# Kernel tuning notes

Measured on AMD Instinct MI355X. Metric: run time of the kernel, lower is better.

## Reference

```python
import jax, jax.numpy as jnp
import numpy as np

B, P, N, C, H, E, HORIZON = 4, 8, 10000, 64, 256, 160000, 4


def setup_inputs() -> dict:
    key = jax.random.key(0)
    ks = jax.random.split(key, 32)
    rn = lambda k, shape, s=0.05: jax.random.normal(k, shape, jnp.float32) * s
    inp = {
        "x_seq": rn(ks[0], (B, P, N, C), 1.0),
        "ei0": jax.random.randint(ks[1], (2, E), 0, N, dtype=jnp.int32),
        "ei1": jax.random.randint(ks[2], (2, E), 0, N, dtype=jnp.int32),
        "Wl0": rn(ks[3], (C, H)), "bl0": jnp.zeros((H,), jnp.float32), "Wr0": rn(ks[4], (C, H)),
        "Wl1": rn(ks[5], (C, H)), "bl1": jnp.zeros((H,), jnp.float32), "Wr1": rn(ks[6], (C, H)),
        "Wp": rn(ks[7], (C, H)), "bp": jnp.zeros((C,), jnp.float32),
    }
    i = 8
    for g in ("g1", "g2", "g3"):
        inp[g + "_Wih"] = rn(ks[i], (3 * H, H)); i += 1
        inp[g + "_Whh"] = rn(ks[i], (3 * H, H)); i += 1
        inp[g + "_bih"] = jnp.zeros((3 * H,), jnp.float32)
        inp[g + "_bhh"] = jnp.zeros((3 * H,), jnp.float32)
    return inp


def _sage(x, src, dst, Wl, bl, Wr, n_nodes):
    # PyG SAGEConv (mean aggr): lin_l(mean_j x_j) + lin_r(x_i); lin_r has no bias.
    agg = jax.ops.segment_sum(x[src], dst, num_segments=n_nodes)  # [n, C]
    cnt = jax.ops.segment_sum(jnp.ones((src.shape[0],), x.dtype), dst, num_segments=n_nodes)
    agg = agg / jnp.maximum(cnt, 1.0)[:, None]
    return agg @ Wl + bl + x @ Wr


def _gru(x, h, Wih, Whh, bih, bhh):
    gi = x @ Wih.T + bih
    gh = h @ Whh.T + bhh
    ir, iz, inn = jnp.split(gi, 3, axis=1)
    hr, hz, hn = jnp.split(gh, 3, axis=1)
    r = jax.nn.sigmoid(ir + hr)
    z = jax.nn.sigmoid(iz + hz)
    n = jnp.tanh(inn + r * hn)
    return (1.0 - z) * n + z * h


def reference(x_seq, ei0, ei1,
              Wl0, bl0, Wr0, Wl1, bl1, Wr1,
              g1_Wih, g1_Whh, g1_bih, g1_bhh,
              g2_Wih, g2_Whh, g2_bih, g2_bhh,
              g3_Wih, g3_Whh, g3_bih, g3_bhh,
              Wp, bp):
    Bn = B * N
    off = (jnp.arange(B) * N).astype(ei0.dtype)
    batch = lambda ei: (ei[:, None, :] + off[None, :, None]).reshape(2, -1)
    b0, b1 = batch(ei0), batch(ei1)

    def step(xt, h1, h2, h3):
        c = (_sage(xt, b0[0], b0[1], Wl0, bl0, Wr0, Bn)
             + _sage(xt, b1[0], b1[1], Wl1, bl1, Wr1, Bn))  # HeteroConv aggr='sum'
        c = jax.nn.relu(c)  # dropout is identity in eval
        h1 = _gru(c, h1, g1_Wih, g1_Whh, g1_bih, g1_bhh)
        h2 = _gru(h1, h2, g2_Wih, g2_Whh, g2_bih, g2_bhh)
        h3 = _gru(h2, h3, g3_Wih, g3_Whh, g3_bih, g3_bhh)
        return h1, h2, h3

    h0 = jnp.zeros((Bn, H), x_seq.dtype)
    xs = jnp.transpose(x_seq, (1, 0, 2, 3)).reshape(P, Bn, C)

    def enc_body(carry, xt):
        return step(xt, *carry), None

    (h1, h2, h3), _ = jax.lax.scan(enc_body, (h0, h0, h0), xs)

    def dec_body(carry, _):
        h1, h2, h3, xd = carry
        h1, h2, h3 = step(xd, h1, h2, h3)
        y = h3 @ Wp.T + bp  # [Bn, C]
        return (h1, h2, h3, y), y

    x_dec = x_seq[:, -1].reshape(Bn, C)
    _, ys = jax.lax.scan(dec_body, (h1, h2, h3, x_dec), None, length=HORIZON)
    # ys: [HORIZON, Bn, C] -> [B, HORIZON, N, C]
    return jnp.transpose(ys.reshape(HORIZON, B, N, C), (1, 0, 2, 3))
```

## Files before the change

kernel.cpp:

```cpp
#include <hip/hip_runtime.h>
#include <hip/hip_bf16.h>
#include <cstdint>

#define B_   4
#define P_   8
#define N_   10000
#define C_   64
#define H_   256
#define E_   160000
#define HOR_ 4
#define BN_  (B_ * N_)
#define MPAD 40064

typedef __bf16 bf16;
typedef __attribute__((ext_vector_type(8))) __bf16 bf16x8;
typedef __attribute__((ext_vector_type(4))) float f32x4;

__device__ __forceinline__ void gl2lds16(const bf16* g, bf16* l) {
    __builtin_amdgcn_global_load_lds(
        (const __attribute__((address_space(1))) void*)g,
        (__attribute__((address_space(3))) void*)l, 16, 0, 0);
}

template <int BIAS, int RELU, int OUTBF, int PROJ>
__global__ __launch_bounds__(256) void gemm_k(
    const bf16* __restrict__ A, const bf16* __restrict__ Bt,
    void* __restrict__ Cp, const float* __restrict__ bias,
    int K, int Nn, int tstep)
{
    __shared__ __align__(16) bf16 As[128 * 32];
    __shared__ __align__(16) bf16 Bs[128 * 32];

    const int tid  = threadIdx.x;
    const int m0   = blockIdx.y * 128;
    const int n0   = blockIdx.x * 128;
    const int wave = tid >> 6;
    const int lane = tid & 63;
    const int wm   = (wave >> 1) << 6;
    const int wn   = (wave & 1) << 6;
    const int lr   = lane & 15;
    const int kg   = lane >> 4;

    f32x4 acc[4][4] = {};

    const int r0 = tid >> 2;
    const int k0 = (tid & 3) << 3;

    for (int kk = 0; kk < K; kk += 32) {
        const bf16* ga = A  + (size_t)(m0 + r0) * K + kk + k0;
        const bf16* gb = Bt + (size_t)(n0 + r0) * K + kk + k0;
        gl2lds16(ga,                  As + tid * 8);
        gl2lds16(ga + 64 * (size_t)K, As + 2048 + tid * 8);
        gl2lds16(gb,                  Bs + tid * 8);
        gl2lds16(gb + 64 * (size_t)K, Bs + 2048 + tid * 8);
        __syncthreads();

        bf16x8 af[4], bfv[4];
#pragma unroll
        for (int i = 0; i < 4; ++i)
            af[i] = *reinterpret_cast<const bf16x8*>(&As[(wm + i * 16 + lr) * 32 + kg * 8]);
#pragma unroll
        for (int j = 0; j < 4; ++j)
            bfv[j] = *reinterpret_cast<const bf16x8*>(&Bs[(wn + j * 16 + lr) * 32 + kg * 8]);
#pragma unroll
        for (int i = 0; i < 4; ++i)
#pragma unroll
            for (int j = 0; j < 4; ++j)
                acc[i][j] = __builtin_amdgcn_mfma_f32_16x16x32_bf16(af[i], bfv[j], acc[i][j], 0, 0, 0);
        __syncthreads();
    }

#pragma unroll
    for (int i = 0; i < 4; ++i) {
#pragma unroll
        for (int j = 0; j < 4; ++j) {
#pragma unroll
            for (int v = 0; v < 4; ++v) {
                int row = m0 + wm + i * 16 + kg * 4 + v;
                int col = n0 + wn + j * 16 + lr;
                float val = acc[i][j][v];
                if (BIAS) val += bias[col];
                if (RELU) val = fmaxf(val, 0.f);
                if (PROJ) {
                    if (col < C_ && row < BN_) {
                        int b = row / N_, n = row - b * N_;
                        reinterpret_cast<float*>(Cp)[(((size_t)b * HOR_ + tstep) * N_ + n) * C_ + col] = val;
                    }
                } else if (OUTBF) {
                    reinterpret_cast<bf16*>(Cp)[(size_t)row * Nn + col] = (bf16)val;
                } else {
                    reinterpret_cast<float*>(Cp)[(size_t)row * Nn + col] = val;
                }
            }
        }
    }
}

__global__ __launch_bounds__(256, 2) void gru_fused_k(
    const bf16* __restrict__ X, const bf16* __restrict__ Hc,
    bf16* __restrict__ Hn,
    const bf16* __restrict__ Wih, const bf16* __restrict__ Whh,
    const float* __restrict__ bih, const float* __restrict__ bhh)
{
    const int id    = blockIdx.x;
    const int sblk  = id >> 6;
    const int jblk  = (id >> 3) & 7;
    const int slow  = id & 7;
    const int strip = (sblk << 3) | slow;
    if (strip >= 313) return;

    __shared__ __align__(16) bf16 Xs[128 * 32];
    __shared__ __align__(16) bf16 Hs[128 * 32];
    __shared__ __align__(16) bf16 Ws[6 * 32 * 32];

    const int tid  = threadIdx.x;
    const int m0   = strip * 128;
    const int j0   = jblk * 32;
    const int wave = tid >> 6;
    const int lane = tid & 63;
    const int wm   = (wave >> 1) << 6;
    const int wn   = (wave & 1) << 4;
    const int lr   = lane & 15;
    const int kg   = lane >> 4;

    f32x4 acc[4][4] = {};

    const int r0 = tid >> 2;
    const int k0 = (tid & 3) << 3;

    int wgate[3], wrow[3], wk[3];
#pragma unroll
    for (int c = 0; c < 3; ++c) {
        int f = c * 2048 + tid * 8;
        wgate[c] = f >> 10;
        wrow[c]  = (f >> 5) & 31;
        wk[c]    = f & 31;
    }

    for (int kk = 0; kk < 256; kk += 32) {
        gl2lds16(X  + (size_t)(m0 + r0) * 256 + kk + k0,      Xs + tid * 8);
        gl2lds16(X  + (size_t)(m0 + r0 + 64) * 256 + kk + k0, Xs + 2048 + tid * 8);
        gl2lds16(Hc + (size_t)(m0 + r0) * 256 + kk + k0,      Hs + tid * 8);
        gl2lds16(Hc + (size_t)(m0 + r0 + 64) * 256 + kk + k0, Hs + 2048 + tid * 8);
#pragma unroll
        for (int c = 0; c < 3; ++c) {
            int g = wgate[c];
            const bf16* src = (g < 3)
                ? Wih + (size_t)(g * 256 + j0 + wrow[c]) * 256 + kk + wk[c]
                : Whh + (size_t)((g - 3) * 256 + j0 + wrow[c]) * 256 + kk + wk[c];
            gl2lds16(src, Ws + c * 2048 + tid * 8);
        }
        __syncthreads();

        bf16x8 af[4], ah[4], bw[6];
#pragma unroll
        for (int i = 0; i < 4; ++i) {
            af[i] = *reinterpret_cast<const bf16x8*>(&Xs[(wm + i * 16 + lr) * 32 + kg * 8]);
            ah[i] = *reinterpret_cast<const bf16x8*>(&Hs[(wm + i * 16 + lr) * 32 + kg * 8]);
        }
#pragma unroll
        for (int g = 0; g < 6; ++g)
            bw[g] = *reinterpret_cast<const bf16x8*>(&Ws[g * 1024 + (wn + lr) * 32 + kg * 8]);
#pragma unroll
        for (int g = 0; g < 3; ++g)
#pragma unroll
            for (int i = 0; i < 4; ++i)
                acc[g][i] = __builtin_amdgcn_mfma_f32_16x16x32_bf16(af[i], bw[g], acc[g][i], 0, 0, 0);
#pragma unroll
        for (int i = 0; i < 4; ++i)
            acc[0][i] = __builtin_amdgcn_mfma_f32_16x16x32_bf16(ah[i], bw[3], acc[0][i], 0, 0, 0);
#pragma unroll
        for (int i = 0; i < 4; ++i)
            acc[1][i] = __builtin_amdgcn_mfma_f32_16x16x32_bf16(ah[i], bw[4], acc[1][i], 0, 0, 0);
#pragma unroll
        for (int i = 0; i < 4; ++i)
            acc[3][i] = __builtin_amdgcn_mfma_f32_16x16x32_bf16(ah[i], bw[5], acc[3][i], 0, 0, 0);
        __syncthreads();
    }

    const int col = j0 + wn + lr;
    const float b_r  = bih[col]       + bhh[col];
    const float b_z  = bih[256 + col] + bhh[256 + col];
    const float bi_n = bih[512 + col];
    const float bh_n = bhh[512 + col];
#pragma unroll
    for (int i = 0; i < 4; ++i) {
#pragma unroll
        for (int v = 0; v < 4; ++v) {
            int row = m0 + wm + i * 16 + kg * 4 + v;
            float r = __fdividef(1.f, 1.f + __expf(-(acc[0][i][v] + b_r)));
            float z = __fdividef(1.f, 1.f + __expf(-(acc[1][i][v] + b_z)));
            float a = (acc[2][i][v] + bi_n) + r * (acc[3][i][v] + bh_n);
            a = fminf(fmaxf(a, -15.f), 15.f);
            float t2 = __expf(2.f * a);
            float nn = __fdividef(t2 - 1.f, t2 + 1.f);
            float hold = (float)Hc[(size_t)row * 256 + col];
            Hn[(size_t)row * 256 + col] = (bf16)((1.f - z) * nn + z * hold);
        }
    }
}

struct __attribute__((aligned(8))) bf4 { bf16 b[4]; };

__global__ __launch_bounds__(256) void gather_conv_k(
    const float* __restrict__ xbase, long long sB, long long sN,
    const int* __restrict__ rp0, const int* __restrict__ col0,
    const int* __restrict__ rp1, const int* __restrict__ col1,
    bf16* __restrict__ Aconv)
{
    int wid  = (blockIdx.x * 256 + threadIdx.x) >> 6;
    int lane = threadIdx.x & 63;
    if (wid >= BN_) return;
    int b = wid / N_;
    int n = wid - b * N_;
    int eg = lane >> 4;
    int cl = lane & 15;
    const float* xb = xbase + (size_t)b * sB;

    float4 xv = *reinterpret_cast<const float4*>(&xb[(size_t)n * sN + cl * 4]);

    float4 s0 = {0.f, 0.f, 0.f, 0.f};
    int st = rp0[n], en = rp0[n + 1];
    float d0 = fmaxf((float)(en - st), 1.f);
    for (int e = st + eg; e < en; e += 4) {
        const float4 v = *reinterpret_cast<const float4*>(&xb[(size_t)col0[e] * sN + cl * 4]);
        s0.x += v.x; s0.y += v.y; s0.z += v.z; s0.w += v.w;
    }

    float4 s1 = {0.f, 0.f, 0.f, 0.f};
    st = rp1[n]; en = rp1[n + 1];
    float d1 = fmaxf((float)(en - st), 1.f);
    for (int e = st + eg; e < en; e += 4) {
        const float4 v = *reinterpret_cast<const float4*>(&xb[(size_t)col1[e] * sN + cl * 4]);
        s1.x += v.x; s1.y += v.y; s1.z += v.z; s1.w += v.w;
    }

#pragma unroll
    for (int m = 16; m <= 32; m <<= 1) {
        s0.x += __shfl_xor(s0.x, m, 64); s0.y += __shfl_xor(s0.y, m, 64);
        s0.z += __shfl_xor(s0.z, m, 64); s0.w += __shfl_xor(s0.w, m, 64);
        s1.x += __shfl_xor(s1.x, m, 64); s1.y += __shfl_xor(s1.y, m, 64);
        s1.z += __shfl_xor(s1.z, m, 64); s1.w += __shfl_xor(s1.w, m, 64);
    }

    if (eg == 0) {
        float r0 = 1.f / d0, r1 = 1.f / d1;
        bf16* row = Aconv + (size_t)wid * 192;
        bf4 o;
        o.b[0] = (bf16)(s0.x * r0); o.b[1] = (bf16)(s0.y * r0);
        o.b[2] = (bf16)(s0.z * r0); o.b[3] = (bf16)(s0.w * r0);
        *reinterpret_cast<bf4*>(&row[cl * 4]) = o;
        o.b[0] = (bf16)xv.x; o.b[1] = (bf16)xv.y; o.b[2] = (bf16)xv.z; o.b[3] = (bf16)xv.w;
        *reinterpret_cast<bf4*>(&row[64 + cl * 4]) = o;
        o.b[0] = (bf16)(s1.x * r1); o.b[1] = (bf16)(s1.y * r1);
        o.b[2] = (bf16)(s1.z * r1); o.b[3] = (bf16)(s1.w * r1);
        *reinterpret_cast<bf4*>(&row[128 + cl * 4]) = o;
    }
}

__global__ void count_k(const int* __restrict__ ei, int* __restrict__ cnt) {
    int e = blockIdx.x * 256 + threadIdx.x;
    if (e < E_) atomicAdd(&cnt[ei[E_ + e]], 1);
}

__global__ __launch_bounds__(1024) void scan_k(
    const int* __restrict__ cnt, int* __restrict__ rp, int* __restrict__ fill)
{
    __shared__ int sums[1024];
    int t = threadIdx.x;
    const int chunk = 10;
    int lo = t * chunk;
    int hi = lo + chunk; if (hi > N_) hi = N_;
    int s = 0;
    for (int i = lo; i < hi; ++i) s += cnt[i];
    sums[t] = s;
    __syncthreads();
    for (int off = 1; off < 1024; off <<= 1) {
        int u = (t >= off) ? sums[t - off] : 0;
        __syncthreads();
        sums[t] += u;
        __syncthreads();
    }
    int base = (t == 0) ? 0 : sums[t - 1];
    for (int i = lo; i < hi; ++i) { rp[i] = base; fill[i] = base; base += cnt[i]; }
    if (t == 1023) rp[N_] = sums[1023];
}

__global__ void fill_k(const int* __restrict__ ei, int* __restrict__ fill,
                       int* __restrict__ colarr) {
    int e = blockIdx.x * 256 + threadIdx.x;
    if (e < E_) {
        int p = atomicAdd(&fill[ei[E_ + e]], 1);
        colarr[p] = ei[e];
    }
}

__global__ void cvt_bf16_k(const float* __restrict__ s, bf16* __restrict__ d, int n) {
    int i = blockIdx.x * 256 + threadIdx.x;
    if (i < n) d[i] = (bf16)s[i];
}

__global__ void build_conv_bt_k(const float* __restrict__ Wl0, const float* __restrict__ Wr0,
                                const float* __restrict__ Wl1, const float* __restrict__ Wr1,
                                bf16* __restrict__ Bt) {
    int idx = blockIdx.x * 256 + threadIdx.x;
    if (idx >= 256 * 192) return;
    int n = idx / 192, k = idx - n * 192;
    float v;
    if (k < 64)       v = Wl0[k * 256 + n];
    else if (k < 128) v = Wr0[(k - 64) * 256 + n] + Wr1[(k - 64) * 256 + n];
    else              v = Wl1[(k - 128) * 256 + n];
    Bt[idx] = (bf16)v;
}

__global__ void build_conv_bias_k(const float* __restrict__ bl0, const float* __restrict__ bl1,
                                  float* __restrict__ bias) {
    int i = threadIdx.x;
    if (i < 256) bias[i] = bl0[i] + bl1[i];
}

__global__ void build_proj_k(const float* __restrict__ Wp, const float* __restrict__ bp,
                             bf16* __restrict__ Bt, float* __restrict__ bias) {
    int idx = blockIdx.x * 256 + threadIdx.x;
    if (idx < 128 * 256) {
        int n = idx >> 8, k = idx & 255;
        Bt[idx] = (bf16)(n < 64 ? Wp[n * 256 + k] : 0.f);
    }
    if (idx < 128) bias[idx] = (idx < 64) ? bp[idx] : 0.f;
}

extern "C" void kernel_launch(void* const* d_in, const int* in_sizes, int n_in,
                              void* d_out, int out_size, void* d_ws, size_t ws_size,
                              hipStream_t stream)
{
    const float* x_seq = (const float*)d_in[0];
    const int*   ei0   = (const int*)d_in[1];
    const int*   ei1   = (const int*)d_in[2];
    const float* Wl0   = (const float*)d_in[3];
    const float* bl0   = (const float*)d_in[4];
    const float* Wr0   = (const float*)d_in[5];
    const float* Wl1   = (const float*)d_in[6];
    const float* bl1   = (const float*)d_in[7];
    const float* Wr1   = (const float*)d_in[8];
    const float* Wp    = (const float*)d_in[9];
    const float* bp    = (const float*)d_in[10];
    const float* gWih[3], *gWhh[3], *gbih[3], *gbhh[3];
    for (int g = 0; g < 3; ++g) {
        gWih[g] = (const float*)d_in[11 + 4 * g];
        gWhh[g] = (const float*)d_in[12 + 4 * g];
        gbih[g] = (const float*)d_in[13 + 4 * g];
        gbhh[g] = (const float*)d_in[14 + 4 * g];
    }

    char* p = (char*)d_ws;
    auto alloc = [&](size_t bytes) -> char* {
        char* r = p; p += (bytes + 255) & ~(size_t)255; return r;
    };
    bf16*  Aconv  = (bf16*)alloc((size_t)MPAD * 192 * 2);
    bf16*  cbuf   = (bf16*)alloc((size_t)MPAD * 256 * 2);
    bf16*  hbuf[6];
    for (int g = 0; g < 6; ++g) hbuf[g] = (bf16*)alloc((size_t)MPAD * 256 * 2);
    bf16*  wih[3], *whh[3];
    for (int g = 0; g < 3; ++g) {
        wih[g] = (bf16*)alloc((size_t)768 * 256 * 2);
        whh[g] = (bf16*)alloc((size_t)768 * 256 * 2);
    }
    bf16*  btconv = (bf16*)alloc((size_t)256 * 192 * 2);
    float* bconv  = (float*)alloc(256 * 4);
    bf16*  btproj = (bf16*)alloc((size_t)128 * 256 * 2);
    float* bproj  = (float*)alloc(128 * 4);
    int* cnt0  = (int*)alloc(N_ * 4);
    int* cnt1  = (int*)alloc(N_ * 4);
    int* rp0   = (int*)alloc((N_ + 1) * 4);
    int* rp1   = (int*)alloc((N_ + 1) * 4);
    int* fill0 = (int*)alloc((N_ + 1) * 4);
    int* fill1 = (int*)alloc((N_ + 1) * 4);
    int* col0  = (int*)alloc(E_ * 4);
    int* col1  = (int*)alloc(E_ * 4);

    hipMemsetAsync(Aconv, 0, (size_t)MPAD * 192 * 2, stream);
    for (int g = 0; g < 3; ++g)
        hipMemsetAsync(hbuf[g], 0, (size_t)MPAD * 256 * 2, stream);
    hipMemsetAsync(cnt0, 0, N_ * 4, stream);
    hipMemsetAsync(cnt1, 0, N_ * 4, stream);

    for (int g = 0; g < 3; ++g) {
        cvt_bf16_k<<<768, 256, 0, stream>>>(gWih[g], wih[g], 768 * 256);
        cvt_bf16_k<<<768, 256, 0, stream>>>(gWhh[g], whh[g], 768 * 256);
    }
    build_conv_bt_k<<<192, 256, 0, stream>>>(Wl0, Wr0, Wl1, Wr1, btconv);
    build_conv_bias_k<<<1, 256, 0, stream>>>(bl0, bl1, bconv);
    build_proj_k<<<128, 256, 0, stream>>>(Wp, bp, btproj, bproj);

    count_k<<<(E_ + 255) / 256, 256, 0, stream>>>(ei0, cnt0);
    count_k<<<(E_ + 255) / 256, 256, 0, stream>>>(ei1, cnt1);
    scan_k<<<1, 1024, 0, stream>>>(cnt0, rp0, fill0);
    scan_k<<<1, 1024, 0, stream>>>(cnt1, rp1, fill1);
    fill_k<<<(E_ + 255) / 256, 256, 0, stream>>>(ei0, fill0, col0);
    fill_k<<<(E_ + 255) / 256, 256, 0, stream>>>(ei1, fill1, col1);

    bf16 *hc[3] = { hbuf[0], hbuf[1], hbuf[2] };
    bf16 *hn[3] = { hbuf[3], hbuf[4], hbuf[5] };

    auto do_conv = [&](const float* xb, long long sB, long long sN) {
        gather_conv_k<<<10000, 256, 0, stream>>>(xb, sB, sN, rp0, col0, rp1, col1, Aconv);
        gemm_k<1, 1, 1, 0><<<dim3(2, 313, 1), 256, 0, stream>>>(
            Aconv, btconv, cbuf, bconv, 192, 256, 0);
    };
    auto do_grus = [&]() {
        gru_fused_k<<<2560, 256, 0, stream>>>(
            cbuf, hc[0], hn[0], wih[0], whh[0], gbih[0], gbhh[0]);
        gru_fused_k<<<2560, 256, 0, stream>>>(
            hn[0], hc[1], hn[1], wih[1], whh[1], gbih[1], gbhh[1]);
        gru_fused_k<<<2560, 256, 0, stream>>>(
            hn[1], hc[2], hn[2], wih[2], whh[2], gbih[2], gbhh[2]);
        for (int g = 0; g < 3; ++g) { bf16* t = hc[g]; hc[g] = hn[g]; hn[g] = t; }
    };

    for (int ps = 0; ps < P_; ++ps) {
        do_conv(x_seq + (size_t)ps * N_ * C_, (long long)P_ * N_ * C_, C_);
        do_grus();
    }

    float* out = (float*)d_out;
    for (int t = 0; t < HOR_; ++t) {
        if (t > 0)
            do_conv(out + (size_t)(t - 1) * N_ * C_, (long long)HOR_ * N_ * C_, C_);
        do_grus();
        gemm_k<1, 0, 0, 1><<<dim3(1, 313, 1), 256, 0, stream>>>(
            hc[2], btproj, out, bproj, 256, 128, t);
    }
}
```

Before: 2.770 ms.

## Prepack GRU weights into MFMA fragment layout and load them directly to registers

GRU weights are repacked once at setup into a per-wave, per-k-step layout that matches the MFMA B-fragment order. The GRU kernel then reads each wave's six weight fragments straight from global memory into registers with coalesced 16-byte loads, and no longer stages them through LDS. This cuts LDS traffic and shared-memory footprint, and the X and H fragment loads are split to lower register pressure. The cost is global or L2 weight loads that are not shared across the waves of a block and sit inside the k-loop without prefetch.

```diff
diff --git a/kernel.cpp b/kernel.cpp
--- a/kernel.cpp
+++ b/kernel.cpp
@@ -99,7 +99,7 @@
 __global__ __launch_bounds__(256, 2) void gru_fused_k(
     const bf16* __restrict__ X, const bf16* __restrict__ Hc,
     bf16* __restrict__ Hn,
-    const bf16* __restrict__ Wih, const bf16* __restrict__ Whh,
+    const bf16* __restrict__ Wpk,
     const float* __restrict__ bih, const float* __restrict__ bhh)
 {
     const int id    = blockIdx.x;
@@ -111,7 +111,6 @@
 
     __shared__ __align__(16) bf16 Xs[128 * 32];
     __shared__ __align__(16) bf16 Hs[128 * 32];
-    __shared__ __align__(16) bf16 Ws[6 * 32 * 32];
 
     const int tid  = threadIdx.x;
     const int m0   = strip * 128;
@@ -120,6 +119,7 @@
     const int lane = tid & 63;
     const int wm   = (wave >> 1) << 6;
     const int wn   = (wave & 1) << 4;
+    const int wv   = wave & 1;
     const int lr   = lane & 15;
     const int kg   = lane >> 4;
 
@@ -128,53 +128,53 @@
     const int r0 = tid >> 2;
     const int k0 = (tid & 3) << 3;
 
-    int wgate[3], wrow[3], wk[3];
-#pragma unroll
-    for (int c = 0; c < 3; ++c) {
-        int f = c * 2048 + tid * 8;
-        wgate[c] = f >> 10;
-        wrow[c]  = (f >> 5) & 31;
-        wk[c]    = f & 31;
-    }
-
-    for (int kk = 0; kk < 256; kk += 32) {
+    const bf16* wb = Wpk + (size_t)(jblk * 2 + wv) * 24576 + lane * 8;
+
+    for (int it = 0; it < 8; ++it) {
+        const int kk = it * 32;
         gl2lds16(X  + (size_t)(m0 + r0) * 256 + kk + k0,      Xs + tid * 8);
         gl2lds16(X  + (size_t)(m0 + r0 + 64) * 256 + kk + k0, Xs + 2048 + tid * 8);
         gl2lds16(Hc + (size_t)(m0 + r0) * 256 + kk + k0,      Hs + tid * 8);
         gl2lds16(Hc + (size_t)(m0 + r0 + 64) * 256 + kk + k0, Hs + 2048 + tid * 8);
-#pragma unroll
-        for (int c = 0; c < 3; ++c) {
-            int g = wgate[c];
-            const bf16* src = (g < 3)
-                ? Wih + (size_t)(g * 256 + j0 + wrow[c]) * 256 + kk + wk[c]
-                : Whh + (size_t)((g - 3) * 256 + j0 + wrow[c]) * 256 + kk + wk[c];
-            gl2lds16(src, Ws + c * 2048 + tid * 8);
+        const bf16* wit = wb + it * 3072;
+        bf16x8 w0 = *reinterpret_cast<const bf16x8*>(&wit[0]);
+        bf16x8 w1 = *reinterpret_cast<const bf16x8*>(&wit[512]);
+        bf16x8 w2 = *reinterpret_cast<const bf16x8*>(&wit[1024]);
+        bf16x8 w3 = *reinterpret_cast<const bf16x8*>(&wit[1536]);
+        bf16x8 w4 = *reinterpret_cast<const bf16x8*>(&wit[2048]);
+        bf16x8 w5 = *reinterpret_cast<const bf16x8*>(&wit[2560]);
+        __syncthreads();
+
+        {
+            bf16x8 fa[4];
+#pragma unroll
+            for (int i = 0; i < 4; ++i)
+                fa[i] = *reinterpret_cast<const bf16x8*>(&Xs[(wm + i * 16 + lr) * 32 + kg * 8]);
+#pragma unroll
+            for (int i = 0; i < 4; ++i)
+                acc[0][i] = __builtin_amdgcn_mfma_f32_16x16x32_bf16(fa[i], w0, acc[0][i], 0, 0, 0);
+#pragma unroll
+            for (int i = 0; i < 4; ++i)
+                acc[1][i] = __builtin_amdgcn_mfma_f32_16x16x32_bf16(fa[i], w1, acc[1][i], 0, 0, 0);
+#pragma unroll
+            for (int i = 0; i < 4; ++i)
+                acc[2][i] = __builtin_amdgcn_mfma_f32_16x16x32_bf16(fa[i], w2, acc[2][i], 0, 0, 0);
         }
-        __syncthreads();
-
-        bf16x8 af[4], ah[4], bw[6];
-#pragma unroll
-        for (int i = 0; i < 4; ++i) {
-            af[i] = *reinterpret_cast<const bf16x8*>(&Xs[(wm + i * 16 + lr) * 32 + kg * 8]);
-            ah[i] = *reinterpret_cast<const bf16x8*>(&Hs[(wm + i * 16 + lr) * 32 + kg * 8]);
+        {
+            bf16x8 fh[4];
+#pragma unroll
+            for (int i = 0; i < 4; ++i)
+                fh[i] = *reinterpret_cast<const bf16x8*>(&Hs[(wm + i * 16 + lr) * 32 + kg * 8]);
+#pragma unroll
+            for (int i = 0; i < 4; ++i)
+                acc[0][i] = __builtin_amdgcn_mfma_f32_16x16x32_bf16(fh[i], w3, acc[0][i], 0, 0, 0);
+#pragma unroll
+            for (int i = 0; i < 4; ++i)
+                acc[1][i] = __builtin_amdgcn_mfma_f32_16x16x32_bf16(fh[i], w4, acc[1][i], 0, 0, 0);
+#pragma unroll
+            for (int i = 0; i < 4; ++i)
+                acc[3][i] = __builtin_amdgcn_mfma_f32_16x16x32_bf16(fh[i], w5, acc[3][i], 0, 0, 0);
         }
-#pragma unroll
-        for (int g = 0; g < 6; ++g)
-            bw[g] = *reinterpret_cast<const bf16x8*>(&Ws[g * 1024 + (wn + lr) * 32 + kg * 8]);
-#pragma unroll
-        for (int g = 0; g < 3; ++g)
-#pragma unroll
-            for (int i = 0; i < 4; ++i)
-                acc[g][i] = __builtin_amdgcn_mfma_f32_16x16x32_bf16(af[i], bw[g], acc[g][i], 0, 0, 0);
-#pragma unroll
-        for (int i = 0; i < 4; ++i)
-            acc[0][i] = __builtin_amdgcn_mfma_f32_16x16x32_bf16(ah[i], bw[3], acc[0][i], 0, 0, 0);
-#pragma unroll
-        for (int i = 0; i < 4; ++i)
-            acc[1][i] = __builtin_amdgcn_mfma_f32_16x16x32_bf16(ah[i], bw[4], acc[1][i], 0, 0, 0);
-#pragma unroll
-        for (int i = 0; i < 4; ++i)
-            acc[3][i] = __builtin_amdgcn_mfma_f32_16x16x32_bf16(ah[i], bw[5], acc[3][i], 0, 0, 0);
         __syncthreads();
     }
 
@@ -295,9 +295,21 @@
     }
 }
 
-__global__ void cvt_bf16_k(const float* __restrict__ s, bf16* __restrict__ d, int n) {
-    int i = blockIdx.x * 256 + threadIdx.x;
-    if (i < n) d[i] = (bf16)s[i];
+__global__ void pack_w_k(const float* __restrict__ Wih, const float* __restrict__ Whh,
+                         bf16* __restrict__ out) {
+    int idx = blockIdx.x * 256 + threadIdx.x;
+    if (idx >= 6 * 256 * 256) return;
+    int e    = idx & 7;
+    int lane = (idx >> 3) & 63;
+    int rest = idx >> 9;
+    int g    = rest % 6;
+    int it   = (rest / 6) & 7;
+    int wj   = rest / 48;
+    int row  = (wj >> 1) * 32 + (wj & 1) * 16 + (lane & 15);
+    int k    = it * 32 + (lane >> 4) * 8 + e;
+    float v  = (g < 3) ? Wih[(g * 256 + row) * 256 + k]
+                       : Whh[((g - 3) * 256 + row) * 256 + k];
+    out[idx] = (bf16)v;
 }
 
 __global__ void build_conv_bt_k(const float* __restrict__ Wl0, const float* __restrict__ Wr0,
@@ -360,11 +372,9 @@
     bf16*  cbuf   = (bf16*)alloc((size_t)MPAD * 256 * 2);
     bf16*  hbuf[6];
     for (int g = 0; g < 6; ++g) hbuf[g] = (bf16*)alloc((size_t)MPAD * 256 * 2);
-    bf16*  wih[3], *whh[3];
-    for (int g = 0; g < 3; ++g) {
-        wih[g] = (bf16*)alloc((size_t)768 * 256 * 2);
-        whh[g] = (bf16*)alloc((size_t)768 * 256 * 2);
-    }
+    bf16*  wpk[3];
+    for (int g = 0; g < 3; ++g)
+        wpk[g] = (bf16*)alloc((size_t)6 * 256 * 256 * 2);
     bf16*  btconv = (bf16*)alloc((size_t)256 * 192 * 2);
     float* bconv  = (float*)alloc(256 * 4);
     bf16*  btproj = (bf16*)alloc((size_t)128 * 256 * 2);
@@ -384,10 +394,8 @@
     hipMemsetAsync(cnt0, 0, N_ * 4, stream);
     hipMemsetAsync(cnt1, 0, N_ * 4, stream);
 
-    for (int g = 0; g < 3; ++g) {
-        cvt_bf16_k<<<768, 256, 0, stream>>>(gWih[g], wih[g], 768 * 256);
-        cvt_bf16_k<<<768, 256, 0, stream>>>(gWhh[g], whh[g], 768 * 256);
-    }
+    for (int g = 0; g < 3; ++g)
+        pack_w_k<<<1536, 256, 0, stream>>>(gWih[g], gWhh[g], wpk[g]);
     build_conv_bt_k<<<192, 256, 0, stream>>>(Wl0, Wr0, Wl1, Wr1, btconv);
     build_conv_bias_k<<<1, 256, 0, stream>>>(bl0, bl1, bconv);
     build_proj_k<<<128, 256, 0, stream>>>(Wp, bp, btproj, bproj);
@@ -409,11 +417,11 @@
     };
     auto do_grus = [&]() {
         gru_fused_k<<<2560, 256, 0, stream>>>(
-            cbuf, hc[0], hn[0], wih[0], whh[0], gbih[0], gbhh[0]);
+            cbuf, hc[0], hn[0], wpk[0], gbih[0], gbhh[0]);
         gru_fused_k<<<2560, 256, 0, stream>>>(
-            hn[0], hc[1], hn[1], wih[1], whh[1], gbih[1], gbhh[1]);
+            hn[0], hc[1], hn[1], wpk[1], gbih[1], gbhh[1]);
         gru_fused_k<<<2560, 256, 0, stream>>>(
-            hn[1], hc[2], hn[2], wih[2], whh[2], gbih[2], gbhh[2]);
+            hn[1], hc[2], hn[2], wpk[2], gbih[2], gbhh[2]);
         for (int g = 0; g < 3; ++g) { bf16* t = hc[g]; hc[g] = hn[g]; hn[g] = t; }
     };
 
```

Result: faster. 2.583 ms (-6.7%).
